# Performance work log

Hardware: AMD Instinct MI355X
Metric: run time of the kernel (lower is better)

Reference implementation:

```python
import jax, jax.numpy as jnp
import numpy as np

EPS = 1e-8
EPS12 = 1e-12
TAU = 0.2
IOU_THRESHOLD = 0.5
NEG_INF = -1e9

N, C = 8192, 1024
HID, FGD, CLSD = 256, 64, 128


def setup_inputs() -> dict:
    key = jax.random.key(0)
    ks = jax.random.split(key, 16)
    roi_feats = jax.random.normal(ks[0], (N, C), dtype=jnp.float32)
    # labels in {-1 (ignore), 0 (bg), 1..20 (classes)}
    labels = jax.random.randint(ks[1], (N,), 0, 21, dtype=jnp.int64) - 1
    ious = jax.random.uniform(ks[2], (N,), dtype=jnp.float32)
    s = 0.02
    w1f = jax.random.normal(ks[3], (HID, C), dtype=jnp.float32) * s
    b1f = jnp.zeros((HID,), dtype=jnp.float32)
    w2f = jax.random.normal(ks[4], (FGD, HID), dtype=jnp.float32) * s
    b2f = jnp.zeros((FGD,), dtype=jnp.float32)
    w1c = jax.random.normal(ks[5], (HID, C), dtype=jnp.float32) * s
    b1c = jnp.zeros((HID,), dtype=jnp.float32)
    w2c = jax.random.normal(ks[6], (CLSD, HID), dtype=jnp.float32) * s
    b2c = jnp.zeros((CLSD,), dtype=jnp.float32)
    return {"roi_feats": roi_feats, "labels": labels, "ious": ious,
            "w1f": w1f, "b1f": b1f, "w2f": w2f, "b2f": b2f,
            "w1c": w1c, "b1c": b1c, "w2c": w2c, "b2c": b2c}


def _project_normalize(x, w1, b1, w2, b2):
    h = jax.nn.relu(x @ w1.T + b1)
    z = h @ w2.T + b2
    nrm = jnp.linalg.norm(z, axis=1, keepdims=True)  # F.normalize: z / max(||z||, eps)
    return z / jnp.maximum(nrm, EPS)


def _fg_bg_loss(z_fg, fg_mask, ignore_mask, iou_weight):
    n = z_fg.shape[0]
    anchor = fg_mask & ~ignore_mask
    eye = jnp.eye(n, dtype=bool)
    # pos_mask[i,j] = fg_mask[j] & ~ignore[j], self excluded
    pos = (fg_mask & ~ignore_mask)[None, :] & ~eye  # [N,N]
    sim = (z_fg @ z_fg.T) / TAU
    sim_exp = jnp.exp(sim) * (~eye).astype(sim.dtype)
    denom = sim_exp.sum(axis=1)  # [N]
    numer = jnp.sum(jnp.exp(sim) * pos.astype(sim.dtype), axis=1)  # [N]
    n_pos = pos.sum(axis=1)
    loss_i = -jnp.log((numer + EPS) / (denom + EPS))
    valid = anchor & (n_pos > 0)
    w = iou_weight
    num = jnp.sum(jnp.where(valid, loss_i * w, 0.0))
    den = jnp.sum(jnp.where(valid, w, 0.0)) + EPS
    return num / den


def _class_supcon_loss(z_cls, labels, fg_mask, ignore_mask, iou_weight):
    n = z_cls.shape[0]
    anchor = fg_mask & ~ignore_mask
    eye = jnp.eye(n, dtype=bool)
    valid_den = ~eye & ~ignore_mask[None, :]  # [N,N]
    # pos[i,j]: same label, j not ignored, labels[j] != 0, j != i, j valid
    pos = (labels[None, :] == labels[:, None]) & ~ignore_mask[None, :] & (labels[None, :] != 0)
    pos = pos & ~eye & valid_den
    sim = (z_cls @ z_cls.T) / TAU
    logits = jnp.where(valid_den, sim, NEG_INF)
    denom_log = jax.nn.logsumexp(logits, axis=1)  # [N]
    n_pos = pos.sum(axis=1)
    sum_pos = jnp.sum(jnp.where(pos, sim, 0.0), axis=1)
    n_pos_safe = jnp.maximum(n_pos, 1).astype(sim.dtype)
    loss_i = -(sum_pos - n_pos.astype(sim.dtype) * denom_log) / n_pos_safe
    valid = anchor & (n_pos > 0) & valid_den.any(axis=1)
    w = iou_weight
    num = jnp.sum(jnp.where(valid, loss_i * w, 0.0))
    den = jnp.sum(jnp.where(valid, w, 0.0)) + EPS12
    return num / den


def reference(roi_feats, labels, ious, w1f, b1f, w2f, b2f, w1c, b1c, w2c, b2c):
    z_fg = _project_normalize(roi_feats, w1f, b1f, w2f, b2f)
    z_cls = _project_normalize(roi_feats, w1c, b1c, w2c, b2c)
    ignore_mask = labels == -1
    bg_mask = (labels == 0) & ~ignore_mask
    fg_mask = (labels > 0) & ~ignore_mask
    iou_weight = jnp.where(ious > IOU_THRESHOLD, ious, 0.0)
    loss_fg_bg = _fg_bg_loss(z_fg, fg_mask, ignore_mask, iou_weight)
    loss_supcon = _class_supcon_loss(z_cls, labels, fg_mask, ignore_mask, iou_weight)
    # loss_weights = (1.0, 1.0); stacked as [loss_fg_bg, loss_supcon]
    return jnp.stack([loss_fg_bg * 1.0, loss_supcon * 1.0])
```

## Files before the change

### kernel.cpp

```cpp
#include <hip/hip_runtime.h>
#include <hip/hip_bf16.h>
#include <math.h>

#define N_ROI 8192
#define C_IN  1024
#define HIDD  256
#define FGD   64
#define CLSD  128
#define INV_TAU 5.0f

using frag_ab = __attribute__((ext_vector_type(8))) short;
using f32x16  = __attribute__((ext_vector_type(16))) float;

static __device__ __forceinline__ short f32_to_bf16_bits(float f) {
  unsigned u = __builtin_bit_cast(unsigned, f);
  u = (u + 0x7FFFu + ((u >> 16) & 1u)) >> 16;
  return (short)u;
}
static __device__ __forceinline__ float bf16_bits_to_f32(short b) {
  unsigned u = ((unsigned)(unsigned short)b) << 16;
  return __builtin_bit_cast(float, u);
}

__global__ void prep_zero_kernel(float* accum, int* cnt) {
  int t = threadIdx.x;
  if (t < 8) accum[t] = 0.f;
  if (t < 24) cnt[t] = 0;
}

__global__ void prep_stats_kernel(const int* __restrict__ labels,
                                  float* __restrict__ Sfg, float* __restrict__ Pfg,
                                  float* __restrict__ Scls, float* __restrict__ SPc,
                                  float* __restrict__ pfv, float* __restrict__ nimv,
                                  float* __restrict__ ljmv, int* __restrict__ cnt) {
  int i = blockIdx.x * blockDim.x + threadIdx.x;
  if (i >= N_ROI) return;
  Sfg[i] = 0.f; Pfg[i] = 0.f; Scls[i] = 0.f; SPc[i] = 0.f;
  int l = labels[i];
  pfv[i]  = (l > 0)  ? 1.f : 0.f;
  nimv[i] = (l != -1) ? 1.f : 0.f;
  ljmv[i] = (l > 0)  ? (float)l : -7.f;
  int b = l + 1; if (b < 0) b = 0; if (b > 21) b = 21;
  atomicAdd(&cnt[b], 1);
}

__global__ __launch_bounds__(256) void pack_w_kernel(
    const float* __restrict__ w1f, const float* __restrict__ w1c,
    const float* __restrict__ w2f, const float* __restrict__ w2c,
    short* __restrict__ W1pf, short* __restrict__ W1pc,
    short* __restrict__ W2pf, short* __restrict__ W2pc) {
  int b = blockIdx.x;
  const float* src; short* dst; int Ksh; int b0;
  if (b < 128)      { src = w1f; dst = W1pf; Ksh = 10; b0 = 0; }
  else if (b < 256) { src = w1c; dst = W1pc; Ksh = 10; b0 = 128; }
  else if (b < 264) { src = w2f; dst = W2pf; Ksh = 8;  b0 = 256; }
  else              { src = w2c; dst = W2pc; Ksh = 8;  b0 = 264; }
  int K = 1 << Ksh;
  int f = (b - b0) * 256 + threadIdx.x;
  int r = f >> (Ksh - 3);
  int c0 = (f & ((K >> 3) - 1)) << 3;
  float4 v0 = *(const float4*)(src + (size_t)r * K + c0);
  float4 v1 = *(const float4*)(src + (size_t)r * K + c0 + 4);
  union { short s[8]; uint4 v; } o;
  o.s[0] = f32_to_bf16_bits(v0.x); o.s[1] = f32_to_bf16_bits(v0.y);
  o.s[2] = f32_to_bf16_bits(v0.z); o.s[3] = f32_to_bf16_bits(v0.w);
  o.s[4] = f32_to_bf16_bits(v1.x); o.s[5] = f32_to_bf16_bits(v1.y);
  o.s[6] = f32_to_bf16_bits(v1.z); o.s[7] = f32_to_bf16_bits(v1.w);
  ((uint4*)dst)[(size_t)((r >> 5) * (K >> 4) + (c0 >> 4)) * 64 +
                ((c0 >> 3) & 1) * 32 + (r & 31)] = o.v;
}

__global__ __launch_bounds__(256) void gemm1_kernel(
    const float* __restrict__ X,
    const short* __restrict__ W1pf, const short* __restrict__ W1pc,
    const float* __restrict__ b1f, const float* __restrict__ b1c,
    short* __restrict__ Hpf, short* __restrict__ Hpc) {
  __shared__ union {
    uint4 stage[2][1024];
    short tr[4][64][68];
  } sm;
  int tid = threadIdx.x, lane = tid & 63, wv = tid >> 6;
  int Mb = blockIdx.x, Nb = blockIdx.y;
  const short* W1p = blockIdx.z ? W1pc : W1pf;
  const float* b1  = blockIdx.z ? b1c  : b1f;
  short*       Hp  = blockIdx.z ? Hpc  : Hpf;
  int wm = wv >> 1, wn = wv & 1;
  const uint4* W1v = (const uint4*)W1p;

  float4 av[2][2];
  uint4  bv[2];

  auto loadAB = [&](int c) {
    #pragma unroll
    for (int q = 0; q < 2; ++q) {
      int u = q * 256 + tid;
      int row = Mb * 128 + ((u >> 7) << 5) + (u & 31);
      int col = c * 32 + ((u >> 5) & 3) * 8;
      const float* p = X + (size_t)row * C_IN + col;
      av[q][0] = *(const float4*)p;
      av[q][1] = *(const float4*)(p + 4);
      int nt = u >> 7, rem = u & 127;
      bv[q] = W1v[(size_t)((Nb * 4 + nt) * 64 + c * 2) * 64 + rem];
    }
  };
  auto storeStage = [&](int buf) {
    #pragma unroll
    for (int q = 0; q < 2; ++q) {
      int u = q * 256 + tid;
      union { short s[8]; uint4 v; } o;
      o.s[0] = f32_to_bf16_bits(av[q][0].x); o.s[1] = f32_to_bf16_bits(av[q][0].y);
      o.s[2] = f32_to_bf16_bits(av[q][0].z); o.s[3] = f32_to_bf16_bits(av[q][0].w);
      o.s[4] = f32_to_bf16_bits(av[q][1].x); o.s[5] = f32_to_bf16_bits(av[q][1].y);
      o.s[6] = f32_to_bf16_bits(av[q][1].z); o.s[7] = f32_to_bf16_bits(av[q][1].w);
      sm.stage[buf][u] = o.v;
      sm.stage[buf][512 + u] = bv[q];
    }
  };

  f32x16 acc[2][2];
  #pragma unroll
  for (int i = 0; i < 2; ++i)
    #pragma unroll
    for (int j = 0; j < 2; ++j)
      #pragma unroll
      for (int q = 0; q < 16; ++q) acc[i][j][q] = 0.f;

  loadAB(0);
  storeStage(0);
  for (int c = 0; c < 32; ++c) {
    __syncthreads();
    if (c + 1 < 32) loadAB(c + 1);
    int buf = c & 1;
    #pragma unroll
    for (int kc = 0; kc < 2; ++kc) {
      frag_ab a0 = *(const frag_ab*)&sm.stage[buf][(wm * 2 + 0) * 128 + kc * 64 + lane];
      frag_ab a1 = *(const frag_ab*)&sm.stage[buf][(wm * 2 + 1) * 128 + kc * 64 + lane];
      frag_ab b0 = *(const frag_ab*)&sm.stage[buf][512 + (wn * 2 + 0) * 128 + kc * 64 + lane];
      frag_ab b1_ = *(const frag_ab*)&sm.stage[buf][512 + (wn * 2 + 1) * 128 + kc * 64 + lane];
      acc[0][0] = __builtin_amdgcn_mfma_f32_32x32x16_bf16(a0, b0,  acc[0][0], 0, 0, 0);
      acc[0][1] = __builtin_amdgcn_mfma_f32_32x32x16_bf16(a0, b1_, acc[0][1], 0, 0, 0);
      acc[1][0] = __builtin_amdgcn_mfma_f32_32x32x16_bf16(a1, b0,  acc[1][0], 0, 0, 0);
      acc[1][1] = __builtin_amdgcn_mfma_f32_32x32x16_bf16(a1, b1_, acc[1][1], 0, 0, 0);
    }
    if (c + 1 < 32) storeStage((c + 1) & 1);
  }
  __syncthreads();

  int cl_ = lane & 31, h = lane >> 5;
  #pragma unroll
  for (int i = 0; i < 2; ++i)
    #pragma unroll
    for (int j = 0; j < 2; ++j) {
      int cg = Nb * 128 + wn * 64 + j * 32 + cl_;
      float bb = b1[cg];
      #pragma unroll
      for (int g = 0; g < 4; ++g) {
        short4 s4;
        {
          float x0 = fmaxf(acc[i][j][g * 4 + 0] + bb, 0.f);
          float x1 = fmaxf(acc[i][j][g * 4 + 1] + bb, 0.f);
          float x2 = fmaxf(acc[i][j][g * 4 + 2] + bb, 0.f);
          float x3 = fmaxf(acc[i][j][g * 4 + 3] + bb, 0.f);
          s4 = make_short4(f32_to_bf16_bits(x0), f32_to_bf16_bits(x1),
                           f32_to_bf16_bits(x2), f32_to_bf16_bits(x3));
        }
        *(short4*)&sm.tr[wv][j * 32 + cl_][i * 32 + 4 * h + 8 * g] = s4;
      }
    }
  __syncthreads();
  uint4* Hv4 = (uint4*)Hp;
  #pragma unroll
  for (int k = 0; k < 8; ++k) {
    union { short s[8]; uint4 v; } o;
    #pragma unroll
    for (int e = 0; e < 8; ++e) o.s[e] = sm.tr[wv][k * 8 + e][lane];
    int rg = Mb * 128 + wm * 64 + lane;
    int cgk = Nb * 128 + wn * 64 + k * 8;
    Hv4[(size_t)((rg >> 5) * 16 + (cgk >> 4)) * 64 + ((cgk >> 3) & 1) * 32 + (rg & 31)] = o.v;
  }
}

template<int D>
__device__ __forceinline__ void gemm2_head(
    const short* __restrict__ Hp, const short* __restrict__ W2p,
    const float* __restrict__ b2, short* __restrict__ Zr,
    float* __restrict__ tii, short* __restrict__ T, int mb) {
  int lane = threadIdx.x & 63;
  int wv = threadIdx.x >> 6;
  int gt = mb * 4 + wv;
  const frag_ab* Hv = (const frag_ab*)Hp;
  const frag_ab* Wv = (const frag_ab*)W2p;
  constexpr int NT = D / 32;
  frag_ab a[16];
  #pragma unroll
  for (int kc = 0; kc < 16; ++kc) a[kc] = Hv[(size_t)(gt * 16 + kc) * 64 + lane];
  f32x16 acc[NT];
  #pragma unroll
  for (int j = 0; j < NT; ++j)
    #pragma unroll
    for (int q = 0; q < 16; ++q) acc[j][q] = 0.f;
  #pragma unroll
  for (int kc = 0; kc < 16; ++kc)
    #pragma unroll
    for (int j = 0; j < NT; ++j)
      acc[j] = __builtin_amdgcn_mfma_f32_32x32x16_bf16(a[kc], Wv[(j * 16 + kc) * 64 + lane], acc[j], 0, 0, 0);
  int c = lane & 31, h = lane >> 5;
  float bb[NT];
  #pragma unroll
  for (int j = 0; j < NT; ++j) bb[j] = b2[j * 32 + c];
  float s1[16];
  #pragma unroll
  for (int r = 0; r < 16; ++r) {
    s1[r] = 0.f;
    #pragma unroll
    for (int j = 0; j < NT; ++j) {
      float v = acc[j][r] + bb[j];
      s1[r] += v * v;
    }
  }
  #pragma unroll
  for (int r = 0; r < 16; ++r)
    #pragma unroll
    for (int m = 1; m < 32; m <<= 1) s1[r] += __shfl_xor(s1[r], m);
  float s2[16];
  #pragma unroll
  for (int r = 0; r < 16; ++r) s2[r] = 0.f;
  #pragma unroll
  for (int j = 0; j < NT; ++j) {
    int cl = j * 32 + c;
    #pragma unroll
    for (int g = 0; g < 4; ++g) {
      short q0, q1, q2, q3;
      #pragma unroll
      for (int e = 0; e < 4; ++e) {
        int r = g * 4 + e;
        float sc = 1.f / fmaxf(sqrtf(s1[r]), 1e-8f);
        short qb = f32_to_bf16_bits((acc[j][r] + bb[j]) * sc);
        float zf = bf16_bits_to_f32(qb);
        s2[r] += zf * zf;
        if (e == 0) q0 = qb; else if (e == 1) q1 = qb; else if (e == 2) q2 = qb; else q3 = qb;
      }
      *(short4*)&T[cl * 36 + 4 * h + 8 * g] = make_short4(q0, q1, q2, q3);
    }
  }
  #pragma unroll
  for (int r = 0; r < 16; ++r)
    #pragma unroll
    for (int m = 1; m < 32; m <<= 1) s2[r] += __shfl_xor(s2[r], m);
  if (c == 0) {
    #pragma unroll
    for (int r = 0; r < 16; ++r)
      tii[gt * 32 + (r & 3) + 8 * (r >> 2) + 4 * h] = s2[r];
  }
  __syncthreads();
  uint4* Zv = (uint4*)Zr;
  #pragma unroll
  for (int k = 0; k < D / 16; ++k) {
    int c0 = (2 * k + h) * 8;
    union { short s[8]; uint4 u; } o;
    #pragma unroll
    for (int e = 0; e < 8; ++e) o.s[e] = T[(c0 + e) * 36 + c];
    Zv[(size_t)(gt * (D / 16) + k) * 64 + h * 32 + c] = o.u;
  }
}

__global__ __launch_bounds__(256) void gemm2_kernel(
    const short* __restrict__ Hpf, const short* __restrict__ Hpc,
    const short* __restrict__ W2pf, const short* __restrict__ W2pc,
    const float* __restrict__ b2f, const float* __restrict__ b2c,
    short* __restrict__ Zrf, short* __restrict__ Zrc,
    float* __restrict__ tiif, float* __restrict__ tiic) {
  __shared__ short T2[4][128 * 36];
  int wv = threadIdx.x >> 6;
  if ((int)blockIdx.x < 64)
    gemm2_head<64>(Hpf, W2pf, b2f, Zrf, tiif, T2[wv], blockIdx.x);
  else
    gemm2_head<128>(Hpc, W2pc, b2c, Zrc, tiic, T2[wv], blockIdx.x - 64);
}

template<int D, int MODE, int NJT>
__global__ __launch_bounds__(256) void loss_mfma_kernel(
    const short* __restrict__ Zr, const int* __restrict__ labels,
    const float* __restrict__ pfv, const float* __restrict__ nimv,
    const float* __restrict__ ljmv,
    float* __restrict__ Sg, float* __restrict__ Pg) {
  constexpr int KC = D / 16;
  __shared__ __align__(16) short sbuf[2][KC * 512];
  int tid = threadIdx.x, lane = tid & 63, wv = tid >> 6;
  int itile = blockIdx.x * 4 + wv;
  const frag_ab* Zrv = (const frag_ab*)Zr;
  frag_ab a[KC];
  #pragma unroll
  for (int kc = 0; kc < KC; ++kc) a[kc] = Zrv[(itile * KC + kc) * 64 + lane];
  float limf[16];
  if (MODE == 1) {
    #pragma unroll
    for (int r = 0; r < 16; ++r) {
      int row = (r & 3) + 8 * (r >> 2) + 4 * (lane >> 5);
      limf[r] = (float)labels[itile * 32 + row];
    }
  }
  float Ssum[16] = {}, Psum[16] = {};
  int jt0 = blockIdx.y * NJT;
  {
    const uint4* src = (const uint4*)(Zr + (size_t)jt0 * KC * 512);
    uint4* dst = (uint4*)sbuf[0];
    #pragma unroll
    for (int q = 0; q < KC * 64; q += 256) dst[q + tid] = src[q + tid];
  }
  __syncthreads();
  for (int kk = 0; kk < NJT; ++kk) {
    int jt = jt0 + kk;
    if (kk + 1 < NJT) {
      const uint4* src = (const uint4*)(Zr + (size_t)(jt + 1) * KC * 512);
      uint4* dst = (uint4*)sbuf[(kk + 1) & 1];
      #pragma unroll
      for (int q = 0; q < KC * 64; q += 256) dst[q + tid] = src[q + tid];
    }
    const frag_ab* bvf = (const frag_ab*)sbuf[kk & 1];
    int j = jt * 32 + (lane & 31);
    float pf = 0.f, nim = 0.f, ljm = 0.f;
    if (MODE == 0) pf = pfv[j];
    else { nim = nimv[j]; ljm = ljmv[j]; }
    f32x16 acc;
    #pragma unroll
    for (int q = 0; q < 16; ++q) acc[q] = 0.f;
    #pragma unroll
    for (int kc = 0; kc < KC; ++kc)
      acc = __builtin_amdgcn_mfma_f32_32x32x16_bf16(a[kc], bvf[kc * 64 + lane], acc, 0, 0, 0);
    #pragma unroll
    for (int r = 0; r < 16; ++r) {
      if (MODE == 0) {
        float e = __expf(acc[r] * INV_TAU);
        Ssum[r] += e;
        Psum[r] = fmaf(pf, e, Psum[r]);
      } else {
        float t = acc[r] * INV_TAU;
        float e = __expf(t);
        Ssum[r] = fmaf(nim, e, Ssum[r]);
        Psum[r] += (limf[r] == ljm) ? t : 0.f;
      }
    }
    __syncthreads();
  }
  #pragma unroll
  for (int r = 0; r < 16; ++r) {
    float s = Ssum[r], p = Psum[r];
    #pragma unroll
    for (int m = 1; m < 32; m <<= 1) { s += __shfl_xor(s, m); p += __shfl_xor(p, m); }
    if ((lane & 31) == 0) {
      int row = (r & 3) + 8 * (r >> 2) + 4 * (lane >> 5);
      atomicAdd(&Sg[itile * 32 + row], s);
      atomicAdd(&Pg[itile * 32 + row], p);
    }
  }
}

__global__ __launch_bounds__(256) void finalize_kernel(
    const float* __restrict__ Sfg, const float* __restrict__ Pfg,
    const float* __restrict__ Scls, const float* __restrict__ SPc,
    const float* __restrict__ tiif, const float* __restrict__ tiic,
    const int* __restrict__ labels, const float* __restrict__ ious,
    const int* __restrict__ cnt, float* __restrict__ accum) {
  int i = blockIdx.x * 256 + threadIdx.x;
  int l = labels[i];
  float iv = ious[i];
  float w = (iv > 0.5f) ? iv : 0.f;
  int cntP = 0;
  #pragma unroll
  for (int b = 2; b <= 21; ++b) cntP += cnt[b];
  int cntNI = N_ROI - cnt[0];
  bool Pi = (l > 0);
  float numF = 0.f, denF = 0.f, numC = 0.f, denC = 0.f;
  float eF = __expf(INV_TAU * tiif[i]);
  float Sf = Sfg[i] - eF;
  float Pf = Pfg[i] - (Pi ? eF : 0.f);
  int nposF = cntP - (Pi ? 1 : 0);
  if (Pi && nposF > 0) {
    float lossF = logf((Sf + 1e-8f) / (Pf + 1e-8f));
    numF = lossF * w; denF = w;
  }
  float tC = INV_TAU * tiic[i];
  float eC = __expf(tC);
  float Sc = Scls[i] - ((l != -1) ? eC : 0.f);
  float SP = SPc[i] - (Pi ? tC : 0.f);
  int nposC = Pi ? (cnt[l + 1] - 1) : 0;
  bool anyv = (cntNI - ((l != -1) ? 1 : 0)) > 0;
  if (Pi && nposC > 0 && anyv) {
    float lse = logf(Sc);
    float lossC = -(SP - (float)nposC * lse) / fmaxf((float)nposC, 1.f);
    numC = lossC * w; denC = w;
  }
  float v0 = numF, v1 = denF, v2 = numC, v3 = denC;
  #pragma unroll
  for (int m = 1; m < 64; m <<= 1) {
    v0 += __shfl_xor(v0, m); v1 += __shfl_xor(v1, m);
    v2 += __shfl_xor(v2, m); v3 += __shfl_xor(v3, m);
  }
  __shared__ float red[4][4];
  int lane = threadIdx.x & 63, wid = threadIdx.x >> 6;
  if (lane == 0) { red[wid][0]=v0; red[wid][1]=v1; red[wid][2]=v2; red[wid][3]=v3; }
  __syncthreads();
  if (threadIdx.x == 0) {
    float s0=0,s1=0,s2=0,s3=0;
    for (int q = 0; q < 4; ++q) { s0+=red[q][0]; s1+=red[q][1]; s2+=red[q][2]; s3+=red[q][3]; }
    atomicAdd(&accum[0], s0); atomicAdd(&accum[1], s1);
    atomicAdd(&accum[2], s2); atomicAdd(&accum[3], s3);
  }
}

__global__ void write_out_kernel(const float* __restrict__ accum, float* __restrict__ out) {
  out[0] = accum[0] / (accum[1] + 1e-8f);
  out[1] = accum[2] / (accum[3] + 1e-12f);
}

extern "C" void kernel_launch(void* const* d_in, const int* in_sizes, int n_in,
                              void* d_out, int out_size, void* d_ws, size_t ws_size,
                              hipStream_t stream) {
  const float* X    = (const float*)d_in[0];
  const int*  labels= (const int*)d_in[1];
  const float* ious = (const float*)d_in[2];
  const float* w1f  = (const float*)d_in[3];
  const float* b1f  = (const float*)d_in[4];
  const float* w2f  = (const float*)d_in[5];
  const float* b2f  = (const float*)d_in[6];
  const float* w1c  = (const float*)d_in[7];
  const float* b1c  = (const float*)d_in[8];
  const float* w2c  = (const float*)d_in[9];
  const float* b2c  = (const float*)d_in[10];
  float* out = (float*)d_out;

  char* w = (char*)d_ws;
  short* W1pf = (short*)w;            w += 524288;
  short* W1pc = (short*)w;            w += 524288;
  short* W2pf = (short*)w;            w += 32768;
  short* W2pc = (short*)w;            w += 65536;
  short* Hpf  = (short*)w;            w += 4194304;
  short* Hpc  = (short*)w;            w += 4194304;
  short* Zrf  = (short*)w;            w += 1048576;
  short* Zrc  = (short*)w;            w += 2097152;
  float* Sfg  = (float*)w;            w += 32768;
  float* Pfg  = (float*)w;            w += 32768;
  float* Scls = (float*)w;            w += 32768;
  float* SPc  = (float*)w;            w += 32768;
  float* tiif = (float*)w;            w += 32768;
  float* tiic = (float*)w;            w += 32768;
  float* pfv  = (float*)w;            w += 32768;
  float* nimv = (float*)w;            w += 32768;
  float* ljmv = (float*)w;            w += 32768;
  float* accum= (float*)w;            w += 32;
  int*   cnt  = (int*)w;              w += 96;

  prep_zero_kernel<<<1, 64, 0, stream>>>(accum, cnt);
  prep_stats_kernel<<<N_ROI/256, 256, 0, stream>>>(labels, Sfg, Pfg, Scls, SPc,
                                                   pfv, nimv, ljmv, cnt);
  pack_w_kernel<<<280, 256, 0, stream>>>(w1f, w1c, w2f, w2c, W1pf, W1pc, W2pf, W2pc);

  gemm1_kernel<<<dim3(64, 2, 2), 256, 0, stream>>>(X, W1pf, W1pc, b1f, b1c, Hpf, Hpc);
  gemm2_kernel<<<128, 256, 0, stream>>>(Hpf, Hpc, W2pf, W2pc, b2f, b2c,
                                        Zrf, Zrc, tiif, tiic);

  loss_mfma_kernel<FGD, 0, 16><<<dim3(64, 16), 256, 0, stream>>>(Zrf, labels, pfv, nimv, ljmv, Sfg, Pfg);
  loss_mfma_kernel<CLSD, 1, 16><<<dim3(64, 16), 256, 0, stream>>>(Zrc, labels, pfv, nimv, ljmv, Scls, SPc);

  finalize_kernel<<<N_ROI/256, 256, 0, stream>>>(Sfg, Pfg, Scls, SPc, tiif, tiic,
                                                 labels, ious, cnt, accum);
  write_out_kernel<<<1, 1, 0, stream>>>(accum, out);
}
```

Baseline: 229.6 us.

## Restructure GEMM1 tiling, shrink GEMM2 blocks, merge loss kernels, fold output write

GEMM1 now uses 32-row blocks in which each wave holds W1 fragments in registers, loaded straight from global memory, and only the bf16 A tile is staged in shared memory. Both heads are computed in one block, with waves split by head, and the launch grows to 256 blocks. GEMM2 moves to 128-thread blocks with twice as many blocks. The two loss kernels are merged into one launch over blockIdx.z. The final division is done by the last finalize block through an atomic counter, which removes the write_out launch. The aim is fewer launches, more parallel blocks and less shared-memory traffic for B, at the cost of higher register pressure and redundant reads of X and W across blocks.

```diff
diff --git a/kernel.cpp b/kernel.cpp
--- a/kernel.cpp
+++ b/kernel.cpp
@@ -76,107 +76,91 @@
     const float* __restrict__ b1f, const float* __restrict__ b1c,
     short* __restrict__ Hpf, short* __restrict__ Hpc) {
   __shared__ union {
-    uint4 stage[2][1024];
-    short tr[4][64][68];
+    short stageA[2][1024];
+    short T[4][128 * 36];
   } sm;
   int tid = threadIdx.x, lane = tid & 63, wv = tid >> 6;
-  int Mb = blockIdx.x, Nb = blockIdx.y;
-  const short* W1p = blockIdx.z ? W1pc : W1pf;
-  const float* b1  = blockIdx.z ? b1c  : b1f;
-  short*       Hp  = blockIdx.z ? Hpc  : Hpf;
-  int wm = wv >> 1, wn = wv & 1;
-  const uint4* W1v = (const uint4*)W1p;
-
-  float4 av[2][2];
-  uint4  bv[2];
-
-  auto loadAB = [&](int c) {
-    #pragma unroll
-    for (int q = 0; q < 2; ++q) {
-      int u = q * 256 + tid;
-      int row = Mb * 128 + ((u >> 7) << 5) + (u & 31);
-      int col = c * 32 + ((u >> 5) & 3) * 8;
-      const float* p = X + (size_t)row * C_IN + col;
-      av[q][0] = *(const float4*)p;
-      av[q][1] = *(const float4*)(p + 4);
-      int nt = u >> 7, rem = u & 127;
-      bv[q] = W1v[(size_t)((Nb * 4 + nt) * 64 + c * 2) * 64 + rem];
-    }
+  int Mb = blockIdx.x;
+  const short* Wp = (wv >> 1) ? W1pc : W1pf;
+  const float* b1 = (wv >> 1) ? b1c  : b1f;
+  short*       Hp = (wv >> 1) ? Hpc  : Hpf;
+  const uint4* Wv4 = (const uint4*)Wp;
+  int arow = tid >> 3;
+  int ac4  = tid & 7;
+  const float* Xp = X + (size_t)(Mb * 32 + arow) * C_IN + ac4 * 4;
+  int aslot = ((ac4 >> 2) * 64 + ((ac4 >> 1) & 1) * 32 + arow) * 8 + (ac4 & 1) * 4;
+
+  float4 av;
+  frag_ab breg[2][8];
+  f32x16 acc[4];
+  #pragma unroll
+  for (int nt = 0; nt < 4; ++nt)
+    #pragma unroll
+    for (int q = 0; q < 16; ++q) acc[nt][q] = 0.f;
+
+  auto loadA = [&](int c) { av = *(const float4*)(Xp + c * 32); };
+  auto loadB = [&](int c, int s) {
+    #pragma unroll
+    for (int kci = 0; kci < 2; ++kci)
+      #pragma unroll
+      for (int nt = 0; nt < 4; ++nt)
+        breg[s][kci * 4 + nt] =
+            *(const frag_ab*)&Wv4[(size_t)(((wv & 1) * 4 + nt) * 64 + c * 2 + kci) * 64 + lane];
   };
-  auto storeStage = [&](int buf) {
-    #pragma unroll
-    for (int q = 0; q < 2; ++q) {
-      int u = q * 256 + tid;
-      union { short s[8]; uint4 v; } o;
-      o.s[0] = f32_to_bf16_bits(av[q][0].x); o.s[1] = f32_to_bf16_bits(av[q][0].y);
-      o.s[2] = f32_to_bf16_bits(av[q][0].z); o.s[3] = f32_to_bf16_bits(av[q][0].w);
-      o.s[4] = f32_to_bf16_bits(av[q][1].x); o.s[5] = f32_to_bf16_bits(av[q][1].y);
-      o.s[6] = f32_to_bf16_bits(av[q][1].z); o.s[7] = f32_to_bf16_bits(av[q][1].w);
-      sm.stage[buf][u] = o.v;
-      sm.stage[buf][512 + u] = bv[q];
-    }
+  auto storeA = [&](int buf) {
+    *(short4*)&sm.stageA[buf][aslot] =
+        make_short4(f32_to_bf16_bits(av.x), f32_to_bf16_bits(av.y),
+                    f32_to_bf16_bits(av.z), f32_to_bf16_bits(av.w));
   };
-
-  f32x16 acc[2][2];
-  #pragma unroll
-  for (int i = 0; i < 2; ++i)
-    #pragma unroll
-    for (int j = 0; j < 2; ++j)
-      #pragma unroll
-      for (int q = 0; q < 16; ++q) acc[i][j][q] = 0.f;
-
-  loadAB(0);
-  storeStage(0);
-  for (int c = 0; c < 32; ++c) {
+  auto domfma = [&](int buf, int bank) {
+    frag_ab a0 = *(const frag_ab*)&sm.stageA[buf][(0 * 64 + lane) * 8];
+    frag_ab a1 = *(const frag_ab*)&sm.stageA[buf][(1 * 64 + lane) * 8];
+    #pragma unroll
+    for (int nt = 0; nt < 4; ++nt)
+      acc[nt] = __builtin_amdgcn_mfma_f32_32x32x16_bf16(a0, breg[bank][nt], acc[nt], 0, 0, 0);
+    #pragma unroll
+    for (int nt = 0; nt < 4; ++nt)
+      acc[nt] = __builtin_amdgcn_mfma_f32_32x32x16_bf16(a1, breg[bank][4 + nt], acc[nt], 0, 0, 0);
+  };
+
+  loadA(0); loadB(0, 0); storeA(0);
+  __syncthreads();
+  for (int c = 0; c < 32; c += 2) {
+    if (c + 1 < 32) { loadA(c + 1); loadB(c + 1, 1); }
+    domfma(0, 0);
+    if (c + 1 < 32) storeA(1);
     __syncthreads();
-    if (c + 1 < 32) loadAB(c + 1);
-    int buf = c & 1;
-    #pragma unroll
-    for (int kc = 0; kc < 2; ++kc) {
-      frag_ab a0 = *(const frag_ab*)&sm.stage[buf][(wm * 2 + 0) * 128 + kc * 64 + lane];
-      frag_ab a1 = *(const frag_ab*)&sm.stage[buf][(wm * 2 + 1) * 128 + kc * 64 + lane];
-      frag_ab b0 = *(const frag_ab*)&sm.stage[buf][512 + (wn * 2 + 0) * 128 + kc * 64 + lane];
-      frag_ab b1_ = *(const frag_ab*)&sm.stage[buf][512 + (wn * 2 + 1) * 128 + kc * 64 + lane];
-      acc[0][0] = __builtin_amdgcn_mfma_f32_32x32x16_bf16(a0, b0,  acc[0][0], 0, 0, 0);
-      acc[0][1] = __builtin_amdgcn_mfma_f32_32x32x16_bf16(a0, b1_, acc[0][1], 0, 0, 0);
-      acc[1][0] = __builtin_amdgcn_mfma_f32_32x32x16_bf16(a1, b0,  acc[1][0], 0, 0, 0);
-      acc[1][1] = __builtin_amdgcn_mfma_f32_32x32x16_bf16(a1, b1_, acc[1][1], 0, 0, 0);
-    }
-    if (c + 1 < 32) storeStage((c + 1) & 1);
-  }
-  __syncthreads();
-
-  int cl_ = lane & 31, h = lane >> 5;
-  #pragma unroll
-  for (int i = 0; i < 2; ++i)
-    #pragma unroll
-    for (int j = 0; j < 2; ++j) {
-      int cg = Nb * 128 + wn * 64 + j * 32 + cl_;
-      float bb = b1[cg];
-      #pragma unroll
-      for (int g = 0; g < 4; ++g) {
-        short4 s4;
-        {
-          float x0 = fmaxf(acc[i][j][g * 4 + 0] + bb, 0.f);
-          float x1 = fmaxf(acc[i][j][g * 4 + 1] + bb, 0.f);
-          float x2 = fmaxf(acc[i][j][g * 4 + 2] + bb, 0.f);
-          float x3 = fmaxf(acc[i][j][g * 4 + 3] + bb, 0.f);
-          s4 = make_short4(f32_to_bf16_bits(x0), f32_to_bf16_bits(x1),
-                           f32_to_bf16_bits(x2), f32_to_bf16_bits(x3));
-        }
-        *(short4*)&sm.tr[wv][j * 32 + cl_][i * 32 + 4 * h + 8 * g] = s4;
-      }
-    }
+    if (c + 2 < 32) { loadA(c + 2); loadB(c + 2, 0); }
+    domfma(1, 1);
+    if (c + 2 < 32) storeA(0);
+    __syncthreads();
+  }
+  int cl31 = lane & 31, h = lane >> 5;
+  short* T = sm.T[wv];
+  #pragma unroll
+  for (int nt = 0; nt < 4; ++nt) {
+    int colLocal = nt * 32 + cl31;
+    float bb = b1[(wv & 1) * 128 + colLocal];
+    #pragma unroll
+    for (int g = 0; g < 4; ++g) {
+      float x0 = fmaxf(acc[nt][g * 4 + 0] + bb, 0.f);
+      float x1 = fmaxf(acc[nt][g * 4 + 1] + bb, 0.f);
+      float x2 = fmaxf(acc[nt][g * 4 + 2] + bb, 0.f);
+      float x3 = fmaxf(acc[nt][g * 4 + 3] + bb, 0.f);
+      *(short4*)&T[colLocal * 36 + 4 * h + 8 * g] =
+          make_short4(f32_to_bf16_bits(x0), f32_to_bf16_bits(x1),
+                      f32_to_bf16_bits(x2), f32_to_bf16_bits(x3));
+    }
+  }
   __syncthreads();
   uint4* Hv4 = (uint4*)Hp;
   #pragma unroll
   for (int k = 0; k < 8; ++k) {
     union { short s[8]; uint4 v; } o;
-    #pragma unroll
-    for (int e = 0; e < 8; ++e) o.s[e] = sm.tr[wv][k * 8 + e][lane];
-    int rg = Mb * 128 + wm * 64 + lane;
-    int cgk = Nb * 128 + wn * 64 + k * 8;
-    Hv4[(size_t)((rg >> 5) * 16 + (cgk >> 4)) * 64 + ((cgk >> 3) & 1) * 32 + (rg & 31)] = o.v;
+    int c0 = k * 16 + h * 8;
+    #pragma unroll
+    for (int e = 0; e < 8; ++e) o.s[e] = T[(c0 + e) * 36 + cl31];
+    Hv4[(size_t)(Mb * 16 + (wv & 1) * 8 + k) * 64 + h * 32 + cl31] = o.v;
   }
 }
 
@@ -184,10 +168,8 @@
 __device__ __forceinline__ void gemm2_head(
     const short* __restrict__ Hp, const short* __restrict__ W2p,
     const float* __restrict__ b2, short* __restrict__ Zr,
-    float* __restrict__ tii, short* __restrict__ T, int mb) {
+    float* __restrict__ tii, short* __restrict__ T, int gt) {
   int lane = threadIdx.x & 63;
-  int wv = threadIdx.x >> 6;
-  int gt = mb * 4 + wv;
   const frag_ab* Hv = (const frag_ab*)Hp;
   const frag_ab* Wv = (const frag_ab*)W2p;
   constexpr int NT = D / 32;
@@ -264,28 +246,28 @@
   }
 }
 
-__global__ __launch_bounds__(256) void gemm2_kernel(
+__global__ __launch_bounds__(128) void gemm2_kernel(
     const short* __restrict__ Hpf, const short* __restrict__ Hpc,
     const short* __restrict__ W2pf, const short* __restrict__ W2pc,
     const float* __restrict__ b2f, const float* __restrict__ b2c,
     short* __restrict__ Zrf, short* __restrict__ Zrc,
     float* __restrict__ tiif, float* __restrict__ tiic) {
-  __shared__ short T2[4][128 * 36];
+  __shared__ short T2[2][128 * 36];
   int wv = threadIdx.x >> 6;
-  if ((int)blockIdx.x < 64)
-    gemm2_head<64>(Hpf, W2pf, b2f, Zrf, tiif, T2[wv], blockIdx.x);
+  int b = blockIdx.x;
+  if (b < 128)
+    gemm2_head<64>(Hpf, W2pf, b2f, Zrf, tiif, T2[wv], b * 2 + wv);
   else
-    gemm2_head<128>(Hpc, W2pc, b2c, Zrc, tiic, T2[wv], blockIdx.x - 64);
+    gemm2_head<128>(Hpc, W2pc, b2c, Zrc, tiic, T2[wv], (b - 128) * 2 + wv);
 }
 
 template<int D, int MODE, int NJT>
-__global__ __launch_bounds__(256) void loss_mfma_kernel(
-    const short* __restrict__ Zr, const int* __restrict__ labels,
+__device__ __forceinline__ void loss_body(
+    short* sbuf, const short* __restrict__ Zr, const int* __restrict__ labels,
     const float* __restrict__ pfv, const float* __restrict__ nimv,
     const float* __restrict__ ljmv,
     float* __restrict__ Sg, float* __restrict__ Pg) {
   constexpr int KC = D / 16;
-  __shared__ __align__(16) short sbuf[2][KC * 512];
   int tid = threadIdx.x, lane = tid & 63, wv = tid >> 6;
   int itile = blockIdx.x * 4 + wv;
   const frag_ab* Zrv = (const frag_ab*)Zr;
@@ -304,7 +286,7 @@
   int jt0 = blockIdx.y * NJT;
   {
     const uint4* src = (const uint4*)(Zr + (size_t)jt0 * KC * 512);
-    uint4* dst = (uint4*)sbuf[0];
+    uint4* dst = (uint4*)sbuf;
     #pragma unroll
     for (int q = 0; q < KC * 64; q += 256) dst[q + tid] = src[q + tid];
   }
@@ -313,11 +295,11 @@
     int jt = jt0 + kk;
     if (kk + 1 < NJT) {
       const uint4* src = (const uint4*)(Zr + (size_t)(jt + 1) * KC * 512);
-      uint4* dst = (uint4*)sbuf[(kk + 1) & 1];
+      uint4* dst = (uint4*)(sbuf + ((kk + 1) & 1) * KC * 512);
       #pragma unroll
       for (int q = 0; q < KC * 64; q += 256) dst[q + tid] = src[q + tid];
     }
-    const frag_ab* bvf = (const frag_ab*)sbuf[kk & 1];
+    const frag_ab* bvf = (const frag_ab*)(sbuf + (kk & 1) * KC * 512);
     int j = jt * 32 + (lane & 31);
     float pf = 0.f, nim = 0.f, ljm = 0.f;
     if (MODE == 0) pf = pfv[j];
@@ -356,12 +338,26 @@
   }
 }
 
+__global__ __launch_bounds__(256) void loss_kernel(
+    const short* __restrict__ Zrf, const short* __restrict__ Zrc,
+    const int* __restrict__ labels,
+    const float* __restrict__ pfv, const float* __restrict__ nimv,
+    const float* __restrict__ ljmv,
+    float* __restrict__ Sfg, float* __restrict__ Pfg,
+    float* __restrict__ Scls, float* __restrict__ SPc) {
+  __shared__ __align__(16) short sbuf[2 * 8 * 512];
+  if (blockIdx.z == 0)
+    loss_body<FGD, 0, 16>(sbuf, Zrf, labels, pfv, nimv, ljmv, Sfg, Pfg);
+  else
+    loss_body<CLSD, 1, 16>(sbuf, Zrc, labels, pfv, nimv, ljmv, Scls, SPc);
+}
+
 __global__ __launch_bounds__(256) void finalize_kernel(
     const float* __restrict__ Sfg, const float* __restrict__ Pfg,
     const float* __restrict__ Scls, const float* __restrict__ SPc,
     const float* __restrict__ tiif, const float* __restrict__ tiic,
     const int* __restrict__ labels, const float* __restrict__ ious,
-    const int* __restrict__ cnt, float* __restrict__ accum) {
+    int* __restrict__ cnt, float* __restrict__ accum, float* __restrict__ out) {
   int i = blockIdx.x * 256 + threadIdx.x;
   int l = labels[i];
   float iv = ious[i];
@@ -406,12 +402,14 @@
     for (int q = 0; q < 4; ++q) { s0+=red[q][0]; s1+=red[q][1]; s2+=red[q][2]; s3+=red[q][3]; }
     atomicAdd(&accum[0], s0); atomicAdd(&accum[1], s1);
     atomicAdd(&accum[2], s2); atomicAdd(&accum[3], s3);
-  }
-}
-
-__global__ void write_out_kernel(const float* __restrict__ accum, float* __restrict__ out) {
-  out[0] = accum[0] / (accum[1] + 1e-8f);
-  out[1] = accum[2] / (accum[3] + 1e-12f);
+    __threadfence();
+    int t = atomicAdd(&cnt[22], 1);
+    if (t == 31) {
+      __threadfence();
+      out[0] = accum[0] / (accum[1] + 1e-8f);
+      out[1] = accum[2] / (accum[3] + 1e-12f);
+    }
+  }
 }
 
 extern "C" void kernel_launch(void* const* d_in, const int* in_sizes, int n_in,
@@ -456,14 +454,13 @@
                                                    pfv, nimv, ljmv, cnt);
   pack_w_kernel<<<280, 256, 0, stream>>>(w1f, w1c, w2f, w2c, W1pf, W1pc, W2pf, W2pc);
 
-  gemm1_kernel<<<dim3(64, 2, 2), 256, 0, stream>>>(X, W1pf, W1pc, b1f, b1c, Hpf, Hpc);
-  gemm2_kernel<<<128, 256, 0, stream>>>(Hpf, Hpc, W2pf, W2pc, b2f, b2c,
+  gemm1_kernel<<<256, 256, 0, stream>>>(X, W1pf, W1pc, b1f, b1c, Hpf, Hpc);
+  gemm2_kernel<<<256, 128, 0, stream>>>(Hpf, Hpc, W2pf, W2pc, b2f, b2c,
                                         Zrf, Zrc, tiif, tiic);
 
-  loss_mfma_kernel<FGD, 0, 16><<<dim3(64, 16), 256, 0, stream>>>(Zrf, labels, pfv, nimv, ljmv, Sfg, Pfg);
-  loss_mfma_kernel<CLSD, 1, 16><<<dim3(64, 16), 256, 0, stream>>>(Zrc, labels, pfv, nimv, ljmv, Scls, SPc);
+  loss_kernel<<<dim3(64, 16, 2), 256, 0, stream>>>(Zrf, Zrc, labels, pfv, nimv, ljmv,
+                                                   Sfg, Pfg, Scls, SPc);
 
   finalize_kernel<<<N_ROI/256, 256, 0, stream>>>(Sfg, Pfg, Scls, SPc, tiif, tiic,
-                                                 labels, ious, cnt, accum);
-  write_out_kernel<<<1, 1, 0, stream>>>(accum, out);
-}
+                                                 labels, ious, cnt, accum, out);
+}
```

Measured after the change: 209.4 us. 8.8% less time.
